# Optimization experiments

Hardware: AMD Instinct MI355X
Metric: run time of the kernel (lower is better)

## Reference

```python
import jax, jax.numpy as jnp
import numpy as np

GRID_SIZE = 5
SPLINE_ORDER = 3
GRID_LO, GRID_HI = -1.0, 1.0
N_BASIS = GRID_SIZE + SPLINE_ORDER  # 8


def make_grid():
    # Extended knot vector as in efficient-kan: grid_size+2*spline_order+1 points
    h = (GRID_HI - GRID_LO) / GRID_SIZE
    return (jnp.arange(-SPLINE_ORDER, GRID_SIZE + SPLINE_ORDER + 1, dtype=jnp.float32) * h + GRID_LO)  # (12,)


def b_splines(x, grid):
    # Cox-de Boor recursion; x: (...,) -> (..., N_BASIS)
    xg = x[..., None]
    bases = ((xg >= grid[:-1]) & (xg < grid[1:])).astype(x.dtype)
    for k in range(1, SPLINE_ORDER + 1):
        left = (xg - grid[: -(k + 1)]) / (grid[k:-1] - grid[: -(k + 1)]) * bases[..., :-1]
        right = (grid[k + 1:] - xg) / (grid[k + 1:] - grid[1:-k]) * bases[..., 1:]
        bases = left + right
    return bases


def extract_patches3(x):
    # x: (B, C, H, W) -> (B, C, 9, H, W); 3x3 kernel, stride 1, padding 1
    B, C, H, W = x.shape
    xp = jnp.pad(x, ((0, 0), (0, 0), (1, 1), (1, 1)))
    return jnp.stack([xp[:, :, di:di + H, dj:dj + W]
                      for di in range(3) for dj in range(3)], axis=2)


def kan_conv(x, base_w, spline_w, scaler, grid):
    # One KANLinear(9 -> 1) per (out_ch, in_ch) pair, summed over in_ch.
    p = extract_patches3(x)                          # (B, Cin, 9, H, W)
    base = jnp.einsum('biphw,oip->bohw', jax.nn.silu(p), base_w)
    basis = b_splines(p, grid)                       # (B, Cin, 9, H, W, G)
    sw = spline_w * scaler[..., None]                # standalone spline scaler
    spl = jnp.einsum('biphwg,oipg->bohw', basis, sw)
    return base + spl


def maxpool2(x):
    B, C, H, W = x.shape
    return x.reshape(B, C, H // 2, 2, W // 2, 2).max(axis=(3, 5))


def setup_inputs() -> dict:
    key = jax.random.key(0)
    ks = jax.random.split(key, 7)
    return {
        'x': jax.random.normal(ks[0], (2048, 1, 28, 28), dtype=jnp.float32),
        'base_w1': jax.random.normal(ks[1], (2, 1, 9), dtype=jnp.float32) * 0.3,
        'spline_w1': jax.random.normal(ks[2], (2, 1, 9, 8), dtype=jnp.float32) * 0.1,
        'scaler1': jax.random.normal(ks[3], (2, 1, 9), dtype=jnp.float32) * 0.3 + 1.0,
        'base_w2': jax.random.normal(ks[4], (2, 2, 9), dtype=jnp.float32) * 0.3,
        'spline_w2': jax.random.normal(ks[5], (2, 2, 9, 8), dtype=jnp.float32) * 0.1,
        'scaler2': jax.random.normal(ks[6], (2, 2, 9), dtype=jnp.float32) * 0.3 + 1.0,
    }


def reference(x, base_w1, spline_w1, scaler1, base_w2, spline_w2, scaler2):
    grid = make_grid()
    h = maxpool2(kan_conv(x, base_w1, spline_w1, scaler1, grid))   # (B, 2, 14, 14)
    h = maxpool2(kan_conv(h, base_w2, spline_w2, scaler2, grid))   # (B, 2, 7, 7)
    return h.reshape(h.shape[0], -1)                               # (B, 98)
```

## Files before the change

kernel.cpp:

```cpp
#include <hip/hip_runtime.h>
#include <math.h>

typedef _Float16 half_t;
typedef _Float16 h2 __attribute__((ext_vector_type(2)));
typedef unsigned int uint;

#define TPB 256

__device__ __forceinline__ uint pack_h2f(float a, float b) {
  half_t ha = (half_t)a, hb = (half_t)b;
  unsigned short ua = __builtin_bit_cast(unsigned short, ha);
  unsigned short ub = __builtin_bit_cast(unsigned short, hb);
  return (uint)ua | ((uint)ub << 16);
}

__device__ __forceinline__ float dot8(uint d0, uint d1, uint d2, uint d3,
                                      float sv, const uint* __restrict__ w,
                                      float acc) {
  acc = fmaf(sv, __uint_as_float(w[4]), acc);
#if __has_builtin(__builtin_amdgcn_fdot2)
  acc = __builtin_amdgcn_fdot2(__builtin_bit_cast(h2, d0), __builtin_bit_cast(h2, w[0]), acc, false);
  acc = __builtin_amdgcn_fdot2(__builtin_bit_cast(h2, d1), __builtin_bit_cast(h2, w[1]), acc, false);
  acc = __builtin_amdgcn_fdot2(__builtin_bit_cast(h2, d2), __builtin_bit_cast(h2, w[2]), acc, false);
  acc = __builtin_amdgcn_fdot2(__builtin_bit_cast(h2, d3), __builtin_bit_cast(h2, w[3]), acc, false);
#else
  uint dd[4] = {d0, d1, d2, d3};
#pragma unroll
  for (int k = 0; k < 4; ++k) {
    h2 f = __builtin_bit_cast(h2, dd[k]);
    h2 wv = __builtin_bit_cast(h2, w[k]);
    acc = fmaf((float)f.x, (float)wv.x, acc);
    acc = fmaf((float)f.y, (float)wv.y, acc);
  }
#endif
  return acc;
}

__device__ __forceinline__ void feat_store(float x, uint* __restrict__ slot) {
  float e = __expf(-x);
  float silu = x * __builtin_amdgcn_rcpf(1.0f + e);
  float s = fmaf(x, 2.5f, 5.5f);
  float sf = floorf(s);
  float t = s - sf;
  int i = (int)sf;
  float omt = 1.0f - t;
  float t2 = t * t;
  float B[4];
  B[0] = (1.0f / 6.0f) * omt * omt * omt;
  B[3] = (1.0f / 6.0f) * t2 * t;
  B[1] = fmaf(0.5f * t, t2, 2.0f / 3.0f - t2);
  B[2] = 1.0f - B[0] - B[1] - B[3];
  *(uint2*)(slot) = make_uint2(0u, 0u);
  *(uint2*)(slot + 2) = make_uint2(0u, 0u);
  slot[4] = __float_as_uint(silu);
  half_t* hp = (half_t*)slot;
  const int p = i - 3;
#pragma unroll
  for (int k = 0; k < 4; ++k) {
    int g = p + k;
    int tgt = ((uint)g < 8u) ? g : 10;
    hp[tgt] = (half_t)B[k];
  }
}

__global__ void pack_w(const float* __restrict__ bw1, const float* __restrict__ sw1,
                       const float* __restrict__ sc1, const float* __restrict__ bw2,
                       const float* __restrict__ sw2, const float* __restrict__ sc2,
                       uint* __restrict__ W) {
  const int t = threadIdx.x;
  if (t < 18) {
    const float scv = sc1[t];
    uint* dst = W + t * 5;
#pragma unroll
    for (int j = 0; j < 4; ++j)
      dst[j] = pack_h2f(sw1[t * 8 + 2 * j] * scv, sw1[t * 8 + 2 * j + 1] * scv);
    dst[4] = __float_as_uint(bw1[t]);
  } else if (t < 54) {
    const int q = t - 18;
    const float scv = sc2[q];
    uint* dst = W + 90 + q * 5;
#pragma unroll
    for (int j = 0; j < 4; ++j)
      dst[j] = pack_h2f(sw2[q * 8 + 2 * j] * scv, sw2[q * 8 + 2 * j + 1] * scv);
    dst[4] = __float_as_uint(bw2[q]);
  }
}

__global__ __launch_bounds__(TPB, 5) void kan_fwd(
    const float* __restrict__ x, const uint* __restrict__ W,
    float* __restrict__ out)
{
  __shared__ __align__(16) uint lds[5400 + 2352];
  uint* F1 = lds;
  uint* F2 = lds + 5400;
  float* P = (float*)lds;

  const int tid = threadIdx.x;
  const float* xb = x + (size_t)blockIdx.x * 784;

  for (int ii = tid; ii < 900; ii += TPB) {
    int r = ii / 30, c = ii % 30;
    bool inter = ((uint)(r - 1) < 28u) && ((uint)(c - 1) < 28u);
    int xi = (r - 1) * 28 + (c - 1);
    xi = min(max(xi, 0), 783);
    float xv = xb[xi];
    xv = inter ? xv : 0.0f;
    feat_store(xv, F1 + ii * 6);
  }
  __syncthreads();

  if (tid < 196) {
    const int ph = tid / 14, pw = tid % 14;
    float acc[2][4];
#pragma unroll
    for (int o = 0; o < 2; ++o)
#pragma unroll
      for (int q = 0; q < 4; ++q) acc[o][q] = 0.0f;
#pragma unroll
    for (int r = 0; r < 4; ++r) {
#pragma unroll
      for (int c = 0; c < 4; ++c) {
        const uint* sl = F1 + ((2 * ph + r) * 30 + (2 * pw + c)) * 6;
        uint2 a = *(const uint2*)sl;
        uint2 bq = *(const uint2*)(sl + 2);
        float sv = __uint_as_float(sl[4]);
#pragma unroll
        for (int dh = 0; dh < 2; ++dh) {
          if (r - dh < 0 || r - dh > 2) continue;
#pragma unroll
          for (int dw = 0; dw < 2; ++dw) {
            if (c - dw < 0 || c - dw > 2) continue;
            const int tap = (r - dh) * 3 + (c - dw);
#pragma unroll
            for (int o = 0; o < 2; ++o)
              acc[o][dh * 2 + dw] =
                  dot8(a.x, a.y, bq.x, bq.y, sv, W + (o * 9 + tap) * 5, acc[o][dh * 2 + dw]);
          }
        }
      }
    }
#pragma unroll
    for (int o = 0; o < 2; ++o) {
      float m = fmaxf(fmaxf(acc[o][0], acc[o][1]), fmaxf(acc[o][2], acc[o][3]));
      feat_store(m, F2 + (o * 196 + tid) * 6);
    }
  }
  __syncthreads();

  {
    const int wid = __builtin_amdgcn_readfirstlane(tid >> 6);
    const int lane = tid & 63;
    const uint F0d1 = pack_h2f(1.0f / 48.0f, 23.0f / 48.0f);
    const uint F0d2 = pack_h2f(23.0f / 48.0f, 1.0f / 48.0f);
    if (lane < 49) {
      const int ci = wid & 1;
      const int ph = lane / 7, pw = lane % 7;
      float pa[4] = {0.0f, 0.0f, 0.0f, 0.0f};
#pragma unroll
      for (int r = 0; r < 4; ++r) {
#pragma unroll
        for (int c = 0; c < 4; ++c) {
          int row = 2 * ph + r - 1, col = 2 * pw + c - 1;
          bool ok = ((uint)row < 14u) && ((uint)col < 14u);
          int rcl = min(max(row, 0), 13), ccl = min(max(col, 0), 13);
          const uint* sl = F2 + (ci * 196 + rcl * 14 + ccl) * 6;
          uint2 a = *(const uint2*)sl;
          uint2 bq = *(const uint2*)(sl + 2);
          float sv = ok ? __uint_as_float(sl[4]) : 0.0f;
          uint d0 = ok ? a.x : 0u;
          uint d1 = ok ? a.y : F0d1;
          uint d2 = ok ? bq.x : F0d2;
          uint d3 = ok ? bq.y : 0u;
#pragma unroll
          for (int dh = 0; dh < 2; ++dh) {
            if (r - dh < 0 || r - dh > 2) continue;
#pragma unroll
            for (int dw = 0; dw < 2; ++dw) {
              if (c - dw < 0 || c - dw > 2) continue;
              const int tap = (r - dh) * 3 + (c - dw);
              pa[dh * 2 + dw] =
                  dot8(d0, d1, d2, d3, sv, W + 90 + (wid * 9 + tap) * 5, pa[dh * 2 + dw]);
            }
          }
        }
      }
      *(float4*)&P[(wid * 49 + lane) * 4] = make_float4(pa[0], pa[1], pa[2], pa[3]);
    }
  }
  __syncthreads();

  if (tid < 98) {
    const int o = tid / 49, pos = tid % 49;
    const float4 p0 = *(const float4*)&P[((o * 2 + 0) * 49 + pos) * 4];
    const float4 p1 = *(const float4*)&P[((o * 2 + 1) * 49 + pos) * 4];
    float m = fmaxf(fmaxf(p0.x + p1.x, p0.y + p1.y), fmaxf(p0.z + p1.z, p0.w + p1.w));
    out[(size_t)blockIdx.x * 98 + tid] = m;
  }
}

extern "C" void kernel_launch(void* const* d_in, const int* in_sizes, int n_in,
                              void* d_out, int out_size, void* d_ws, size_t ws_size,
                              hipStream_t stream) {
  const float* x   = (const float*)d_in[0];
  const float* bw1 = (const float*)d_in[1];
  const float* sw1 = (const float*)d_in[2];
  const float* sc1 = (const float*)d_in[3];
  const float* bw2 = (const float*)d_in[4];
  const float* sw2 = (const float*)d_in[5];
  const float* sc2 = (const float*)d_in[6];
  float* out = (float*)d_out;
  uint* W = (uint*)d_ws;
  const int B = in_sizes[0] / 784;
  pack_w<<<1, 64, 0, stream>>>(bw1, sw1, sc1, bw2, sw2, sc2, W);
  kan_fwd<<<B, TPB, 0, stream>>>(x, W, out);
}
```

Before: 85.52 us.

## Stage weights in LDS, reorder feature columns, and store silu as fp16

Packed weights are copied into LDS and reorganised so both output channels' weights for a tap sit next to each other, and each base weight is held in an fp16 pair so silu can go through fdot2. Feature columns in LDS are stored even/odd-split, which spreads neighbouring lanes' accesses across banks and cuts bank conflicts. Stage-1 work is spread over 4 waves of 49 lanes, and the basis reads are hoisted into registers and reused across taps. Storing silu in fp16 lowers precision and the added arrays raise register pressure.

Result: slower. 88.80 us (+3.8%).

```diff
diff --git a/kernel.cpp b/kernel.cpp
--- a/kernel.cpp
+++ b/kernel.cpp
@@ -14,25 +14,22 @@
   return (uint)ua | ((uint)ub << 16);
 }
 
-__device__ __forceinline__ float dot8(uint d0, uint d1, uint d2, uint d3,
-                                      float sv, const uint* __restrict__ w,
-                                      float acc) {
-  acc = fmaf(sv, __uint_as_float(w[4]), acc);
+__device__ __forceinline__ float fdot2f(uint f, uint w, float acc) {
 #if __has_builtin(__builtin_amdgcn_fdot2)
-  acc = __builtin_amdgcn_fdot2(__builtin_bit_cast(h2, d0), __builtin_bit_cast(h2, w[0]), acc, false);
-  acc = __builtin_amdgcn_fdot2(__builtin_bit_cast(h2, d1), __builtin_bit_cast(h2, w[1]), acc, false);
-  acc = __builtin_amdgcn_fdot2(__builtin_bit_cast(h2, d2), __builtin_bit_cast(h2, w[2]), acc, false);
-  acc = __builtin_amdgcn_fdot2(__builtin_bit_cast(h2, d3), __builtin_bit_cast(h2, w[3]), acc, false);
+  return __builtin_amdgcn_fdot2(__builtin_bit_cast(h2, f),
+                                __builtin_bit_cast(h2, w), acc, false);
 #else
-  uint dd[4] = {d0, d1, d2, d3};
-#pragma unroll
-  for (int k = 0; k < 4; ++k) {
-    h2 f = __builtin_bit_cast(h2, dd[k]);
-    h2 wv = __builtin_bit_cast(h2, w[k]);
-    acc = fmaf((float)f.x, (float)wv.x, acc);
-    acc = fmaf((float)f.y, (float)wv.y, acc);
-  }
+  h2 a = __builtin_bit_cast(h2, f), b = __builtin_bit_cast(h2, w);
+  acc = fmaf((float)a.x, (float)b.x, acc);
+  return fmaf((float)a.y, (float)b.y, acc);
 #endif
+}
+
+__device__ __forceinline__ float dot8b(uint2 fa, uint2 fb, uint4 w, float acc) {
+  acc = fdot2f(fa.x, w.x, acc);
+  acc = fdot2f(fa.y, w.y, acc);
+  acc = fdot2f(fb.x, w.z, acc);
+  acc = fdot2f(fb.y, w.w, acc);
   return acc;
 }
 
@@ -42,23 +39,21 @@
   float s = fmaf(x, 2.5f, 5.5f);
   float sf = floorf(s);
   float t = s - sf;
-  int i = (int)sf;
-  float omt = 1.0f - t;
-  float t2 = t * t;
+  int p = (int)sf - 3;
+  float omt = 1.0f - t, t2 = t * t;
   float B[4];
   B[0] = (1.0f / 6.0f) * omt * omt * omt;
   B[3] = (1.0f / 6.0f) * t2 * t;
   B[1] = fmaf(0.5f * t, t2, 2.0f / 3.0f - t2);
   B[2] = 1.0f - B[0] - B[1] - B[3];
-  *(uint2*)(slot) = make_uint2(0u, 0u);
+  *(uint2*)slot = make_uint2(0u, 0u);
   *(uint2*)(slot + 2) = make_uint2(0u, 0u);
-  slot[4] = __float_as_uint(silu);
+  slot[4] = (uint)__builtin_bit_cast(unsigned short, (half_t)silu);
   half_t* hp = (half_t*)slot;
-  const int p = i - 3;
 #pragma unroll
   for (int k = 0; k < 4; ++k) {
     int g = p + k;
-    int tgt = ((uint)g < 8u) ? g : 10;
+    int tgt = ((uint)g < 8u) ? g : 9;
     hp[tgt] = (half_t)B[k];
   }
 }
@@ -69,61 +64,74 @@
                        uint* __restrict__ W) {
   const int t = threadIdx.x;
   if (t < 18) {
+    const int o = t / 9, tap = t - o * 9;
     const float scv = sc1[t];
-    uint* dst = W + t * 5;
 #pragma unroll
     for (int j = 0; j < 4; ++j)
-      dst[j] = pack_h2f(sw1[t * 8 + 2 * j] * scv, sw1[t * 8 + 2 * j + 1] * scv);
-    dst[4] = __float_as_uint(bw1[t]);
+      W[tap * 8 + o * 4 + j] =
+          pack_h2f(sw1[t * 8 + 2 * j] * scv, sw1[t * 8 + 2 * j + 1] * scv);
+    W[72 + tap * 2 + o] = pack_h2f(bw1[t], 0.0f);
   } else if (t < 54) {
     const int q = t - 18;
+    const int wid = q / 9, tap = q - wid * 9;
     const float scv = sc2[q];
-    uint* dst = W + 90 + q * 5;
 #pragma unroll
     for (int j = 0; j < 4; ++j)
-      dst[j] = pack_h2f(sw2[q * 8 + 2 * j] * scv, sw2[q * 8 + 2 * j + 1] * scv);
-    dst[4] = __float_as_uint(bw2[q]);
-  }
-}
+      W[96 + wid * 36 + tap * 4 + j] =
+          pack_h2f(sw2[q * 8 + 2 * j] * scv, sw2[q * 8 + 2 * j + 1] * scv);
+    W[240 + wid * 9 + tap] = pack_h2f(bw2[q], 0.0f);
+  }
+}
+
+#define REMAP30(col) (((col) >> 1) + ((col) & 1) * 15)
+#define REMAP14(col) (((col) >> 1) + ((col) & 1) * 7)
 
 __global__ __launch_bounds__(TPB, 5) void kan_fwd(
-    const float* __restrict__ x, const uint* __restrict__ W,
+    const float* __restrict__ x, const uint* __restrict__ Wg,
     float* __restrict__ out)
 {
-  __shared__ __align__(16) uint lds[5400 + 2352];
+  __shared__ __align__(16) uint lds[5400 + 2352 + 276];
   uint* F1 = lds;
   uint* F2 = lds + 5400;
+  uint* WL = lds + 7752;
   float* P = (float*)lds;
 
   const int tid = threadIdx.x;
   const float* xb = x + (size_t)blockIdx.x * 784;
 
-  for (int ii = tid; ii < 900; ii += TPB) {
-    int r = ii / 30, c = ii % 30;
-    bool inter = ((uint)(r - 1) < 28u) && ((uint)(c - 1) < 28u);
-    int xi = (r - 1) * 28 + (c - 1);
-    xi = min(max(xi, 0), 783);
+  for (int i = tid; i < 276; i += TPB) WL[i] = Wg[i];
+  for (int s1 = tid; s1 < 900; s1 += TPB) {
+    int row = s1 / 30, m = s1 - row * 30;
+    int col = (m < 15) ? (2 * m) : (2 * (m - 15) + 1);
+    bool inter = ((uint)(row - 1) < 28u) && ((uint)(col - 1) < 28u);
+    int xi = min(max((row - 1) * 28 + (col - 1), 0), 783);
     float xv = xb[xi];
     xv = inter ? xv : 0.0f;
-    feat_store(xv, F1 + ii * 6);
+    feat_store(xv, F1 + s1 * 6);
   }
   __syncthreads();
 
-  if (tid < 196) {
-    const int ph = tid / 14, pw = tid % 14;
+  const int wv = tid >> 6;
+  const int lane = tid & 63;
+
+  if (lane < 49) {
+    const int quad = wv * 49 + lane;
+    const int ph = quad / 14, pw = quad - (quad / 14) * 14;
+    const uint* base = F1 + ((2 * ph) * 30 + pw) * 6;
     float acc[2][4];
 #pragma unroll
     for (int o = 0; o < 2; ++o)
 #pragma unroll
       for (int q = 0; q < 4; ++q) acc[o][q] = 0.0f;
-#pragma unroll
-    for (int r = 0; r < 4; ++r) {
-#pragma unroll
-      for (int c = 0; c < 4; ++c) {
-        const uint* sl = F1 + ((2 * ph + r) * 30 + (2 * pw + c)) * 6;
-        uint2 a = *(const uint2*)sl;
-        uint2 bq = *(const uint2*)(sl + 2);
-        float sv = __uint_as_float(sl[4]);
+
+    uint2 wb[9];
+#pragma unroll
+    for (int tp = 0; tp < 9; ++tp) wb[tp] = *(const uint2*)&WL[72 + tp * 2];
+#pragma unroll
+    for (int r = 0; r < 4; ++r) {
+#pragma unroll
+      for (int c = 0; c < 4; ++c) {
+        uint sil = base[(r * 30 + REMAP30(c)) * 6 + 4];
 #pragma unroll
         for (int dh = 0; dh < 2; ++dh) {
           if (r - dh < 0 || r - dh > 2) continue;
@@ -131,69 +139,123 @@
           for (int dw = 0; dw < 2; ++dw) {
             if (c - dw < 0 || c - dw > 2) continue;
             const int tap = (r - dh) * 3 + (c - dw);
-#pragma unroll
-            for (int o = 0; o < 2; ++o)
-              acc[o][dh * 2 + dw] =
-                  dot8(a.x, a.y, bq.x, bq.y, sv, W + (o * 9 + tap) * 5, acc[o][dh * 2 + dw]);
+            acc[0][dh * 2 + dw] = fdot2f(sil, wb[tap].x, acc[0][dh * 2 + dw]);
+            acc[1][dh * 2 + dw] = fdot2f(sil, wb[tap].y, acc[1][dh * 2 + dw]);
+          }
+        }
+      }
+    }
+
+    uint2 basA[16], basB[16];
+#pragma unroll
+    for (int r = 0; r < 4; ++r) {
+#pragma unroll
+      for (int c = 0; c < 4; ++c) {
+        const uint* sl = base + (r * 30 + REMAP30(c)) * 6;
+        basA[r * 4 + c] = *(const uint2*)sl;
+        basB[r * 4 + c] = *(const uint2*)(sl + 2);
+      }
+    }
+#pragma unroll
+    for (int tr = 0; tr < 3; ++tr) {
+#pragma unroll
+      for (int tc = 0; tc < 3; ++tc) {
+        const int tap = tr * 3 + tc;
+        uint4 w0 = *(const uint4*)&WL[tap * 8];
+        uint4 w1 = *(const uint4*)&WL[tap * 8 + 4];
+#pragma unroll
+        for (int dh = 0; dh < 2; ++dh) {
+#pragma unroll
+          for (int dw = 0; dw < 2; ++dw) {
+            const int px = (tr + dh) * 4 + (tc + dw);
+            acc[0][dh * 2 + dw] = dot8b(basA[px], basB[px], w0, acc[0][dh * 2 + dw]);
+            acc[1][dh * 2 + dw] = dot8b(basA[px], basB[px], w1, acc[1][dh * 2 + dw]);
           }
         }
       }
     }
 #pragma unroll
     for (int o = 0; o < 2; ++o) {
-      float m = fmaxf(fmaxf(acc[o][0], acc[o][1]), fmaxf(acc[o][2], acc[o][3]));
-      feat_store(m, F2 + (o * 196 + tid) * 6);
+      float mx = fmaxf(fmaxf(acc[o][0], acc[o][1]), fmaxf(acc[o][2], acc[o][3]));
+      feat_store(mx, F2 + (o * 196 + ph * 14 + REMAP14(pw)) * 6);
     }
   }
   __syncthreads();
 
-  {
-    const int wid = __builtin_amdgcn_readfirstlane(tid >> 6);
-    const int lane = tid & 63;
+  if (lane < 49) {
+    const int wid = __builtin_amdgcn_readfirstlane(wv);
+    const int ci = wid & 1;
+    const int ph = lane / 7, pw = lane - (lane / 7) * 7;
+    float pa[4] = {0.0f, 0.0f, 0.0f, 0.0f};
+
+    uint wb2[9];
+#pragma unroll
+    for (int tp = 0; tp < 9; ++tp) wb2[tp] = WL[240 + wid * 9 + tp];
+#pragma unroll
+    for (int r = 0; r < 4; ++r) {
+#pragma unroll
+      for (int c = 0; c < 4; ++c) {
+        int row = 2 * ph + r - 1, col = 2 * pw + c - 1;
+        bool ok = ((uint)row < 14u) && ((uint)col < 14u);
+        int rcl = min(max(row, 0), 13), ccl = min(max(col, 0), 13);
+        uint sil = F2[(ci * 196 + rcl * 14 + REMAP14(ccl)) * 6 + 4];
+        sil = ok ? sil : 0u;
+#pragma unroll
+        for (int dh = 0; dh < 2; ++dh) {
+          if (r - dh < 0 || r - dh > 2) continue;
+#pragma unroll
+          for (int dw = 0; dw < 2; ++dw) {
+            if (c - dw < 0 || c - dw > 2) continue;
+            const int tap = (r - dh) * 3 + (c - dw);
+            pa[dh * 2 + dw] = fdot2f(sil, wb2[tap], pa[dh * 2 + dw]);
+          }
+        }
+      }
+    }
+
     const uint F0d1 = pack_h2f(1.0f / 48.0f, 23.0f / 48.0f);
     const uint F0d2 = pack_h2f(23.0f / 48.0f, 1.0f / 48.0f);
-    if (lane < 49) {
-      const int ci = wid & 1;
-      const int ph = lane / 7, pw = lane % 7;
-      float pa[4] = {0.0f, 0.0f, 0.0f, 0.0f};
-#pragma unroll
-      for (int r = 0; r < 4; ++r) {
-#pragma unroll
-        for (int c = 0; c < 4; ++c) {
-          int row = 2 * ph + r - 1, col = 2 * pw + c - 1;
-          bool ok = ((uint)row < 14u) && ((uint)col < 14u);
-          int rcl = min(max(row, 0), 13), ccl = min(max(col, 0), 13);
-          const uint* sl = F2 + (ci * 196 + rcl * 14 + ccl) * 6;
-          uint2 a = *(const uint2*)sl;
-          uint2 bq = *(const uint2*)(sl + 2);
-          float sv = ok ? __uint_as_float(sl[4]) : 0.0f;
-          uint d0 = ok ? a.x : 0u;
-          uint d1 = ok ? a.y : F0d1;
-          uint d2 = ok ? bq.x : F0d2;
-          uint d3 = ok ? bq.y : 0u;
-#pragma unroll
-          for (int dh = 0; dh < 2; ++dh) {
-            if (r - dh < 0 || r - dh > 2) continue;
-#pragma unroll
-            for (int dw = 0; dw < 2; ++dw) {
-              if (c - dw < 0 || c - dw > 2) continue;
-              const int tap = (r - dh) * 3 + (c - dw);
-              pa[dh * 2 + dw] =
-                  dot8(d0, d1, d2, d3, sv, W + 90 + (wid * 9 + tap) * 5, pa[dh * 2 + dw]);
-            }
-          }
-        }
-      }
-      *(float4*)&P[(wid * 49 + lane) * 4] = make_float4(pa[0], pa[1], pa[2], pa[3]);
-    }
+    uint2 basA[16], basB[16];
+#pragma unroll
+    for (int r = 0; r < 4; ++r) {
+#pragma unroll
+      for (int c = 0; c < 4; ++c) {
+        int row = 2 * ph + r - 1, col = 2 * pw + c - 1;
+        bool ok = ((uint)row < 14u) && ((uint)col < 14u);
+        int rcl = min(max(row, 0), 13), ccl = min(max(col, 0), 13);
+        const uint* sl = F2 + (ci * 196 + rcl * 14 + REMAP14(ccl)) * 6;
+        uint2 a = *(const uint2*)sl;
+        uint2 b = *(const uint2*)(sl + 2);
+        basA[r * 4 + c] = make_uint2(ok ? a.x : 0u, ok ? a.y : F0d1);
+        basB[r * 4 + c] = make_uint2(ok ? b.x : F0d2, ok ? b.y : 0u);
+      }
+    }
+#pragma unroll
+    for (int tr = 0; tr < 3; ++tr) {
+#pragma unroll
+      for (int tc = 0; tc < 3; ++tc) {
+        const int tap = tr * 3 + tc;
+        uint4 w = *(const uint4*)&WL[96 + wid * 36 + tap * 4];
+#pragma unroll
+        for (int dh = 0; dh < 2; ++dh) {
+#pragma unroll
+          for (int dw = 0; dw < 2; ++dw) {
+            const int px = (tr + dh) * 4 + (tc + dw);
+            pa[dh * 2 + dw] = dot8b(basA[px], basB[px], w, pa[dh * 2 + dw]);
+          }
+        }
+      }
+    }
+    *(float4*)&P[(wid * 49 + lane) * 4] = make_float4(pa[0], pa[1], pa[2], pa[3]);
   }
   __syncthreads();
 
   if (tid < 98) {
-    const int o = tid / 49, pos = tid % 49;
+    const int o = tid / 49, pos = tid - o * 49;
     const float4 p0 = *(const float4*)&P[((o * 2 + 0) * 49 + pos) * 4];
     const float4 p1 = *(const float4*)&P[((o * 2 + 1) * 49 + pos) * 4];
-    float m = fmaxf(fmaxf(p0.x + p1.x, p0.y + p1.y), fmaxf(p0.z + p1.z, p0.w + p1.w));
+    float m = fmaxf(fmaxf(p0.x + p1.x, p0.y + p1.y),
+                    fmaxf(p0.z + p1.z, p0.w + p1.w));
     out[(size_t)blockIdx.x * 98 + tid] = m;
   }
 }
```
